# Kernel tuning notes

Measured on AMD Instinct MI355X. Metric: run time of the kernel, lower is better.

## Reference

```python
import jax, jax.numpy as jnp
import numpy as np

D_MODEL = 1024
NUM_HEADS = 16
HEAD_DIM = D_MODEL // NUM_HEADS  # 64
# NOTE: the torch module passes scale=attention_head_size (NOT 1/sqrt(dh));
# we reproduce that exact math: scores are MULTIPLIED by head_dim.
SCALE = float(HEAD_DIM)

B, S = 2, 2048


def setup_inputs() -> dict:
    key = jax.random.key(0)
    ks = jax.random.split(key, 6)
    q = jax.random.normal(ks[0], (B, S, D_MODEL), dtype=jnp.float32)
    k = jax.random.normal(ks[1], (B, S, D_MODEL), dtype=jnp.float32)
    v = jax.random.normal(ks[2], (B, S, D_MODEL), dtype=jnp.float32)
    # Linear weights stored as [in, out]; scaled like typical init so the
    # (head_dim-scaled) logits stay numerically sane.
    w_std = 0.02
    Wq = jax.random.normal(ks[3], (D_MODEL, D_MODEL), dtype=jnp.float32) * w_std
    Wk = jax.random.normal(ks[4], (D_MODEL, D_MODEL), dtype=jnp.float32) * w_std
    Wv = jax.random.normal(ks[5], (D_MODEL, D_MODEL), dtype=jnp.float32) * w_std
    return {"q": q, "k": k, "v": v, "Wq": Wq, "Wk": Wk, "Wv": Wv}


def reference(q, k, v, Wq, Wk, Wv):
    Bq, Sq, _ = q.shape
    # QKV projections (qkv_bias=False), split into heads: [B, S, H, dh]
    qh = (q @ Wq).reshape(Bq, Sq, NUM_HEADS, HEAD_DIM)
    kh = (k @ Wk).reshape(Bq, Sq, NUM_HEADS, HEAD_DIM)
    vh = (v @ Wv).reshape(Bq, Sq, NUM_HEADS, HEAD_DIM)
    # Full materialized scores [B, H, Sq, Sk] -- the naive MHA pattern.
    sims = jnp.einsum("bqhd,bkhd->bhqk", qh, kh) * SCALE
    attn = jax.nn.softmax(sims, axis=-1)
    # Second matmul, then merge heads back: [B, S, D]
    out = jnp.einsum("bhqk,bkhd->bqhd", attn, vh).reshape(Bq, Sq, D_MODEL)
    return out
```

## Files before the change

kernel.cpp:

```cpp
#include <hip/hip_runtime.h>
#include <cstdint>
#include <cstddef>

typedef unsigned short u16;
typedef __bf16 bf16x8 __attribute__((ext_vector_type(8)));
typedef float f32x4 __attribute__((ext_vector_type(4)));
typedef unsigned int u32x4 __attribute__((ext_vector_type(4)));
typedef unsigned int u32x2 __attribute__((ext_vector_type(2)));
typedef u16 u16x4 __attribute__((ext_vector_type(4)));

typedef __attribute__((address_space(3))) void lds_void;
typedef __attribute__((address_space(1))) void glb_void;

constexpr float CEXP = 92.33248261689366f;

constexpr size_t XSZ = 4096ull * 1024ull;
constexpr size_t WSZ = 1024ull * 1024ull;
constexpr size_t OFF_XQH = 0;
constexpr size_t OFF_XQL = OFF_XQH + XSZ;
constexpr size_t OFF_XKH = OFF_XQL + XSZ;
constexpr size_t OFF_XKL = OFF_XKH + XSZ;
constexpr size_t OFF_XVH = OFF_XKL + XSZ;
constexpr size_t OFF_XVL = OFF_XVH + XSZ;
constexpr size_t OFF_WQH = OFF_XVL + XSZ;
constexpr size_t OFF_WQL = OFF_WQH + WSZ;
constexpr size_t OFF_WKH = OFF_WQL + WSZ;
constexpr size_t OFF_WKL = OFF_WKH + WSZ;
constexpr size_t OFF_WVH = OFF_WKL + WSZ;
constexpr size_t OFF_WVL = OFF_WVH + WSZ;
constexpr size_t OFF_QH  = OFF_WVL + WSZ;
constexpr size_t OFF_QL  = OFF_QH + XSZ;
constexpr size_t OFF_KH  = OFF_QL + XSZ;
constexpr size_t OFF_KL  = OFF_KH + XSZ;
constexpr size_t OFF_VH  = OFF_KL + XSZ;
constexpr size_t OFF_VT  = OFF_VH + XSZ;

__device__ __forceinline__ u16 f2b(float f) {
  unsigned u = __builtin_bit_cast(unsigned, f);
  return (u16)((u + 0x7FFFu + ((u >> 16) & 1u)) >> 16);
}
__device__ __forceinline__ float b2f(u16 h) {
  return __builtin_bit_cast(float, ((unsigned)h) << 16);
}
__device__ __forceinline__ bf16x8 ld8(const u16* p) {
  return __builtin_bit_cast(bf16x8, *(const u32x4*)p);
}
__device__ __forceinline__ unsigned pk2(float a, float b) {
#if __has_builtin(__builtin_amdgcn_cvt_pk_bf16_f32)
  auto v = __builtin_amdgcn_cvt_pk_bf16_f32(a, b);
  return __builtin_bit_cast(unsigned, v);
#else
  return (unsigned)f2b(a) | ((unsigned)f2b(b) << 16);
#endif
}
__device__ __forceinline__ float ex2(float x) {
#if __has_builtin(__builtin_amdgcn_exp2f)
  return __builtin_amdgcn_exp2f(x);
#else
  return exp2f(x);
#endif
}
__device__ __forceinline__ void glds16(const u16* g, u16* l) {
  __builtin_amdgcn_global_load_lds((const glb_void*)g, (lds_void*)l, 16, 0, 0);
}
__device__ __forceinline__ int swz32(int row, int cg) {
  return row * 32 + ((cg ^ ((row >> 1) & 3)) * 8);
}
__device__ __forceinline__ int swz64(int row, int cg) {
  return row * 64 + ((cg ^ (row & 7)) * 8);
}

__global__ __launch_bounds__(256) void convert_all(const float* __restrict__ q,
                                                   const float* __restrict__ k,
                                                   const float* __restrict__ v,
                                                   const float* __restrict__ Wq,
                                                   const float* __restrict__ Wk,
                                                   const float* __restrict__ Wv,
                                                   u16* __restrict__ ws) {
  __shared__ float tile[32][33];
  int id = blockIdx.x;
  int t = threadIdx.x;
  if (id < 6144) {
    int z = id >> 11, blk = id & 2047;
    const float* in = (z == 0) ? q : (z == 1) ? k : v;
    u16* hi = ws + ((z == 0) ? OFF_XQH : (z == 1) ? OFF_XKH : OFF_XVH);
    u16* lo = ws + ((z == 0) ? OFF_XQL : (z == 1) ? OFF_XKL : OFF_XVL);
    size_t i = ((size_t)blk * 256u + t) * 8u;
    float4 v0 = *(const float4*)(in + i);
    float4 v1 = *(const float4*)(in + i + 4);
    float a[8] = {v0.x, v0.y, v0.z, v0.w, v1.x, v1.y, v1.z, v1.w};
    u16 hv[8], lv[8];
#pragma unroll
    for (int j = 0; j < 8; ++j) {
      u16 hb = f2b(a[j]);
      hv[j] = hb;
      lv[j] = f2b(a[j] - b2f(hb));
    }
    *(u32x4*)(hi + i) = *(const u32x4*)hv;
    if (z != 2) *(u32x4*)(lo + i) = *(const u32x4*)lv;
  } else {
    int r0 = id - 6144;
    int z = r0 >> 10, rem = r0 & 1023;
    const float* W = (z == 0) ? Wq : (z == 1) ? Wk : Wv;
    u16* hiT = ws + ((z == 0) ? OFF_WQH : (z == 1) ? OFF_WKH : OFF_WVH);
    u16* loT = ws + ((z == 0) ? OFF_WQL : (z == 1) ? OFF_WKL : OFF_WVL);
    int n0 = (rem & 31) * 32, k0 = (rem >> 5) * 32;
    int r = t >> 3, c0 = (t & 7) * 4;
    float4 vv = *(const float4*)(W + (size_t)(k0 + r) * 1024 + n0 + c0);
    tile[r][c0] = vv.x; tile[r][c0 + 1] = vv.y; tile[r][c0 + 2] = vv.z; tile[r][c0 + 3] = vv.w;
    __syncthreads();
    u16x4 hv, lv;
#pragma unroll
    for (int j = 0; j < 4; ++j) {
      float x = tile[c0 + j][r];
      u16 hb = f2b(x);
      hv[j] = hb;
      lv[j] = f2b(x - b2f(hb));
    }
    size_t o = (size_t)(n0 + r) * 1024 + k0 + c0;
    *(u16x4*)(hiT + o) = hv;
    if (z != 2) *(u16x4*)(loT + o) = lv;
  }
}

__global__ __launch_bounds__(256, 3) void gemm_qkv(u16* __restrict__ ws) {
  __shared__ u16 smem[16384];
  u16* sAh = smem;
  u16* sAl = smem + 4096;
  u16* sBh = smem + 8192;
  u16* sBl = smem + 12288;
  u16* cbuf = smem;

  int id = blockIdx.x;
  int xcd = id & 7, seq = id >> 3;
  int pair = (seq >> 3) * 8 + xcd;
  int tile_n = seq & 7;
  int z = pair >> 5;
  int tile_m = pair & 31;

  const u16 *Ah, *Al, *Bh, *Bl; u16 *Oh, *Ol; bool split;
  if (z == 0)      { Ah = ws + OFF_XQH; Al = ws + OFF_XQL; Bh = ws + OFF_WQH; Bl = ws + OFF_WQL; Oh = ws + OFF_QH; Ol = ws + OFF_QL; split = true; }
  else if (z == 1) { Ah = ws + OFF_XKH; Al = ws + OFF_XKL; Bh = ws + OFF_WKH; Bl = ws + OFF_WKL; Oh = ws + OFF_KH; Ol = ws + OFF_KL; split = true; }
  else             { Ah = ws + OFF_XVH; Al = nullptr;      Bh = ws + OFF_WVH; Bl = nullptr;      Oh = ws + OFF_VT; Ol = nullptr;    split = false; }
  float oscale = (z == 0) ? CEXP : 1.0f;
  int m0 = tile_m * 128, n0 = tile_n * 128;
  int t = threadIdx.x, lane = t & 63, wave = t >> 6;
  int quad = lane >> 4, l15 = lane & 15;
  int wm = (wave >> 1) * 64, wn = (wave & 1) * 64;
  int rl = lane >> 2, cgl = lane & 3;
  f32x4 acc[4][4] = {};

  size_t gA[2], gB[2]; int lb[2];
#pragma unroll
  for (int i = 0; i < 2; ++i) {
    int row = i * 64 + wave * 16 + rl;
    int gsw = (cgl ^ ((row >> 1) & 3)) * 8;
    gA[i] = (size_t)(m0 + row) * 1024 + gsw;
    gB[i] = (size_t)(n0 + row) * 1024 + gsw;
    lb[i] = i * 2048 + wave * 512;
  }

  for (int kb = 0; kb < 32; ++kb) {
    int k0 = kb * 32;
    __syncthreads();
#pragma unroll
    for (int i = 0; i < 2; ++i) {
      glds16(Ah + gA[i] + k0, &sAh[lb[i]]);
      if (split) glds16(Al + gA[i] + k0, &sAl[lb[i]]);
      glds16(Bh + gB[i] + k0, &sBh[lb[i]]);
      if (split) glds16(Bl + gB[i] + k0, &sBl[lb[i]]);
    }
    __syncthreads();
    bf16x8 afh[4], afl[4];
#pragma unroll
    for (int mt = 0; mt < 4; ++mt) {
      int ra = wm + mt * 16 + l15;
      afh[mt] = ld8(&sAh[swz32(ra, quad)]);
      if (split) afl[mt] = ld8(&sAl[swz32(ra, quad)]);
    }
#pragma unroll
    for (int nt = 0; nt < 4; ++nt) {
      int rb = wn + nt * 16 + l15;
      bf16x8 bfh = ld8(&sBh[swz32(rb, quad)]);
      bf16x8 bfl;
      if (split) bfl = ld8(&sBl[swz32(rb, quad)]);
#pragma unroll
      for (int mt = 0; mt < 4; ++mt) {
        acc[mt][nt] = __builtin_amdgcn_mfma_f32_16x16x32_bf16(afh[mt], bfh, acc[mt][nt], 0, 0, 0);
        if (split) {
          acc[mt][nt] = __builtin_amdgcn_mfma_f32_16x16x32_bf16(afl[mt], bfh, acc[mt][nt], 0, 0, 0);
          acc[mt][nt] = __builtin_amdgcn_mfma_f32_16x16x32_bf16(afh[mt], bfl, acc[mt][nt], 0, 0, 0);
        }
      }
    }
  }
  auto epi_round = [&](u16* dst, bool lo_round) {
#pragma unroll
    for (int mt = 0; mt < 4; ++mt)
#pragma unroll
      for (int nt = 0; nt < 4; ++nt)
#pragma unroll
        for (int r = 0; r < 4; ++r) {
          int row = wm + mt * 16 + quad * 4 + r;
          int col = wn + nt * 16 + l15;
          float v = acc[mt][nt][r] * oscale;
          u16 hb = f2b(v);
          u16 val = lo_round ? f2b(v - b2f(hb)) : hb;
          cbuf[row * 128 + (((col >> 3) ^ (row & 15)) * 8) + (col & 7)] = val;
        }
    __syncthreads();
#pragma unroll
    for (int rr = 0; rr < 2; ++rr) {
      int row = rr * 64 + (t >> 2), seg = t & 3;
      int gm = m0 + row, bb = gm >> 11, s = gm & 2047;
      int hh = (n0 >> 6) + (seg >> 1), d0 = (seg & 1) * 32;
      u16* gp = dst + ((size_t)(bb * 16 + hh) * 2048 + s) * 64 + d0;
#pragma unroll
      for (int i = 0; i < 4; ++i) {
        int phys = (seg * 4 + i) ^ (row & 15);
        *(u32x4*)(gp + i * 8) = *(const u32x4*)(&cbuf[row * 128 + phys * 8]);
      }
    }
  };
  __syncthreads();
  if (split) {
    epi_round(Oh, false);
    __syncthreads();
    epi_round(Ol, true);
  } else {
#pragma unroll
    for (int mt = 0; mt < 4; ++mt)
#pragma unroll
      for (int nt = 0; nt < 4; ++nt)
#pragma unroll
        for (int r = 0; r < 4; ++r) {
          int row = wm + mt * 16 + quad * 4 + r;
          int col = wn + nt * 16 + l15;
          cbuf[row * 128 + (((col >> 3) ^ (row & 15)) * 8) + (col & 7)] =
              f2b(acc[mt][nt][r]);
        }
    __syncthreads();
    int col = t >> 1, sh = t & 1;
    int hg = (n0 + col) >> 6, d = (n0 + col) & 63;
    int bb = m0 >> 11, s0 = m0 & 2047;
#pragma unroll
    for (int part = 0; part < 2; ++part) {
      u16 vals[32];
#pragma unroll
      for (int i = 0; i < 32; ++i) {
        int row = part * 64 + sh * 32 + i;
        vals[i] = cbuf[row * 128 + (((col >> 3) ^ (row & 15)) * 8) + (col & 7)];
      }
      u16* gp = Oh + ((size_t)((bb * 16 + hg) * 64 + d)) * 2048 + s0 + part * 64 + sh * 32;
#pragma unroll
      for (int i = 0; i < 4; ++i)
        *(u32x4*)(gp + i * 8) = *(const u32x4*)(&vals[i * 8]);
    }
  }
}

__global__ __launch_bounds__(256, 4) void attn(const u16* __restrict__ ws,
                                               float* __restrict__ out) {
  __shared__ u16 lkh[64 * 64];
  __shared__ u16 lkl[64 * 64];
  __shared__ u16 lvt[2][64 * 64];
  __shared__ u16 lp[4][16 * 64];
  const u16* Qh = ws + OFF_QH; const u16* Ql = ws + OFF_QL;
  const u16* Kh = ws + OFF_KH; const u16* Kl = ws + OFF_KL;
  const u16* Vt = ws + OFF_VT;
  int id = blockIdx.x;
  int xcd = id & 7, slot = id >> 3;
  int hh = xcd * 4 + (slot >> 5);
  int q0 = (slot & 31) * 64;
  int b = hh >> 4, h = hh & 15;
  int t = threadIdx.x, lane = t & 63, wave = t >> 6;
  int quad = lane >> 4, l15 = lane & 15;
  size_t hb = (size_t)hh * (2048 * 64);
  bf16x8 onesf;
#pragma unroll
  for (int j = 0; j < 8; ++j) onesf[j] = __builtin_bit_cast(__bf16, (u16)0x3F80);
  int qrow = q0 + wave * 16 + l15;
  bf16x8 qfh[2], qfl[2];
#pragma unroll
  for (int ks = 0; ks < 2; ++ks) {
    size_t qo = hb + (size_t)qrow * 64 + ks * 32 + quad * 8;
    qfh[ks] = ld8(Qh + qo);
    qfl[ks] = ld8(Ql + qo);
  }
  float mi = -1e30f;
  f32x4 lsum = {};
  f32x4 o[4] = {};
  int rl = lane >> 3, cgl = lane & 7;

  size_t aK[2], aV[2]; int lb[2];
#pragma unroll
  for (int i = 0; i < 2; ++i) {
    int row = wave * 16 + i * 8 + rl;
    int cgg = cgl ^ (row & 7);
    aK[i] = hb + (size_t)row * 64 + cgg * 8;
    aV[i] = hb + (size_t)row * 2048 + cgg * 8;
    lb[i] = (wave * 16 + i * 8) * 64;
  }
  int soF[2][4];
#pragma unroll
  for (int ks = 0; ks < 2; ++ks)
#pragma unroll
    for (int nt = 0; nt < 4; ++nt)
      soF[ks][nt] = swz64(nt * 16 + l15, ks * 4 + quad);
  int soP[4];
  {
    int r7 = l15 & 7;
#pragma unroll
    for (int nt = 0; nt < 4; ++nt) {
      int c = nt * 2 + (quad >> 1);
      soP[nt] = l15 * 64 + ((c ^ r7) * 8) + (quad & 1) * 4;
    }
  }
  int soPa[2];
#pragma unroll
  for (int ks = 0; ks < 2; ++ks) soPa[ks] = swz64(l15, ks * 4 + quad);
  u16* lpw = &lp[wave][0];

#pragma unroll
  for (int i = 0; i < 2; ++i) {
    glds16(Kh + aK[i], &lkh[lb[i]]);
    glds16(Kl + aK[i], &lkl[lb[i]]);
    glds16(Vt + aV[i], &lvt[0][lb[i]]);
  }
  u32x4 pk_[2], pl_[2], pv_[2];
#pragma unroll
  for (int i = 0; i < 2; ++i) {
    pk_[i] = *(const u32x4*)(Kh + aK[i] + 4096);
    pl_[i] = *(const u32x4*)(Kl + aK[i] + 4096);
    pv_[i] = *(const u32x4*)(Vt + aV[i] + 64);
  }
  __syncthreads();

  for (int kt = 0; kt < 32; ++kt) {
    f32x4 sc[4] = {};
    __builtin_amdgcn_s_setprio(1);
#pragma unroll
    for (int nt = 0; nt < 4; ++nt) {
#pragma unroll
      for (int ks = 0; ks < 2; ++ks) {
        bf16x8 kh_ = ld8(&lkh[soF[ks][nt]]);
        bf16x8 kl_ = ld8(&lkl[soF[ks][nt]]);
        sc[nt] = __builtin_amdgcn_mfma_f32_16x16x32_bf16(kh_, qfh[ks], sc[nt], 0, 0, 0);
        sc[nt] = __builtin_amdgcn_mfma_f32_16x16x32_bf16(kl_, qfh[ks], sc[nt], 0, 0, 0);
        sc[nt] = __builtin_amdgcn_mfma_f32_16x16x32_bf16(kh_, qfl[ks], sc[nt], 0, 0, 0);
      }
    }
    __builtin_amdgcn_s_setprio(0);
    __syncthreads();
    if (kt < 31) {
#pragma unroll
      for (int i = 0; i < 2; ++i) {
        *(u32x4*)(&lkh[lb[i] + lane * 8]) = pk_[i];
        *(u32x4*)(&lkl[lb[i] + lane * 8]) = pl_[i];
        *(u32x4*)(&lvt[(kt + 1) & 1][lb[i] + lane * 8]) = pv_[i];
      }
    }
    __syncthreads();
    if (kt < 30) {
#pragma unroll
      for (int i = 0; i < 2; ++i) {
        pk_[i] = *(const u32x4*)(Kh + aK[i] + (kt + 2) * 4096);
        pl_[i] = *(const u32x4*)(Kl + aK[i] + (kt + 2) * 4096);
        pv_[i] = *(const u32x4*)(Vt + aV[i] + (kt + 2) * 64);
      }
    }
    float t0 = fmaxf(fmaxf(sc[0][0], sc[0][1]), sc[0][2]);
    float t1 = fmaxf(fmaxf(sc[0][3], sc[1][0]), sc[1][1]);
    float t2 = fmaxf(fmaxf(sc[1][2], sc[1][3]), sc[2][0]);
    float t3 = fmaxf(fmaxf(sc[2][1], sc[2][2]), sc[2][3]);
    float t4 = fmaxf(fmaxf(sc[3][0], sc[3][1]), sc[3][2]);
    float mx = fmaxf(fmaxf(fmaxf(t0, t1), fmaxf(t2, t3)), fmaxf(t4, sc[3][3]));
    mx = fmaxf(mx, __shfl_xor(mx, 16));
    mx = fmaxf(mx, __shfl_xor(mx, 32));
    float mi_old = mi;
    unsigned long long live = __ballot(mx > mi_old - 28.0f);
    float mn = fmaxf(mi_old, mx);
    mi = mn;
    if (live) {
      unsigned long long grew = __ballot(mx > mi_old);
#pragma unroll
      for (int nt = 0; nt < 4; ++nt) {
        unsigned u01 = pk2(ex2(sc[nt][0] - mn), ex2(sc[nt][1] - mn));
        unsigned u23 = pk2(ex2(sc[nt][2] - mn), ex2(sc[nt][3] - mn));
        *(u32x2*)(&lpw[soP[nt]]) = u32x2{u01, u23};
      }
      if (grew) {
        float a = ex2(mi_old - mn);
#pragma unroll
        for (int r = 0; r < 4; ++r) {
          lsum[r] *= a;
          o[0][r] *= a; o[1][r] *= a; o[2][r] *= a; o[3][r] *= a;
        }
      }
      asm volatile("s_waitcnt lgkmcnt(0)" ::: "memory");
      bf16x8 pa[2];
#pragma unroll
      for (int ks = 0; ks < 2; ++ks) pa[ks] = ld8(&lpw[soPa[ks]]);
      __builtin_amdgcn_s_setprio(1);
      lsum = __builtin_amdgcn_mfma_f32_16x16x32_bf16(onesf, pa[0], lsum, 0, 0, 0);
      lsum = __builtin_amdgcn_mfma_f32_16x16x32_bf16(onesf, pa[1], lsum, 0, 0, 0);
      const u16* lv = &lvt[kt & 1][0];
#pragma unroll
      for (int nt = 0; nt < 4; ++nt)
#pragma unroll
        for (int ks = 0; ks < 2; ++ks) {
          bf16x8 bv = ld8(&lv[soF[ks][nt]]);
          o[nt] = __builtin_amdgcn_mfma_f32_16x16x32_bf16(bv, pa[ks], o[nt], 0, 0, 0);
        }
      __builtin_amdgcn_s_setprio(0);
    }
  }
  float inv = 1.0f / lsum[0];
  float* op = out + (size_t)(b * 2048 + q0 + wave * 16 + l15) * 1024 + h * 64;
#pragma unroll
  for (int nt = 0; nt < 4; ++nt) {
    f32x4 w;
#pragma unroll
    for (int r = 0; r < 4; ++r) w[r] = o[nt][r] * inv;
    *(f32x4*)(op + nt * 16 + quad * 4) = w;
  }
}

extern "C" void kernel_launch(void* const* d_in, const int* in_sizes, int n_in,
                              void* d_out, int out_size, void* d_ws, size_t ws_size,
                              hipStream_t stream) {
  const float* q  = (const float*)d_in[0];
  const float* k  = (const float*)d_in[1];
  const float* v  = (const float*)d_in[2];
  const float* Wq = (const float*)d_in[3];
  const float* Wk = (const float*)d_in[4];
  const float* Wv = (const float*)d_in[5];
  u16* ws = (u16*)d_ws;
  float* out = (float*)d_out;

  convert_all<<<9216, 256, 0, stream>>>(q, k, v, Wq, Wk, Wv, ws);
  gemm_qkv<<<768, 256, 0, stream>>>(ws);
  attn<<<1024, 256, 0, stream>>>(ws, out);
}
```

Before: 269.9 us.

## Fuse fp32 activation split-to-bf16 conversion into QKV GEMM tile loads

Removes the separate pass that converted q/k/v activations to hi/lo bf16 in workspace. The GEMM now loads fp32 activation tiles directly into LDS, using a new XOR swizzle, and builds the hi/lo bf16 fragments in registers before the MFMAs. This saves the write and re-read of roughly 48 MB of intermediate activations. In exchange, each tile moves twice the fp32 bytes into LDS and the inner loop gains conversion ALU work. Each N tile of the same rows also repeats that conversion.

Result: no change. 272.7 us (+1.0%).

```diff
diff --git a/kernel.cpp b/kernel.cpp
--- a/kernel.cpp
+++ b/kernel.cpp
@@ -16,13 +16,7 @@
 
 constexpr size_t XSZ = 4096ull * 1024ull;
 constexpr size_t WSZ = 1024ull * 1024ull;
-constexpr size_t OFF_XQH = 0;
-constexpr size_t OFF_XQL = OFF_XQH + XSZ;
-constexpr size_t OFF_XKH = OFF_XQL + XSZ;
-constexpr size_t OFF_XKL = OFF_XKH + XSZ;
-constexpr size_t OFF_XVH = OFF_XKL + XSZ;
-constexpr size_t OFF_XVL = OFF_XVH + XSZ;
-constexpr size_t OFF_WQH = OFF_XVL + XSZ;
+constexpr size_t OFF_WQH = 0;
 constexpr size_t OFF_WQL = OFF_WQH + WSZ;
 constexpr size_t OFF_WKH = OFF_WQL + WSZ;
 constexpr size_t OFF_WKL = OFF_WKH + WSZ;
@@ -32,8 +26,7 @@
 constexpr size_t OFF_QL  = OFF_QH + XSZ;
 constexpr size_t OFF_KH  = OFF_QL + XSZ;
 constexpr size_t OFF_KL  = OFF_KH + XSZ;
-constexpr size_t OFF_VH  = OFF_KL + XSZ;
-constexpr size_t OFF_VT  = OFF_VH + XSZ;
+constexpr size_t OFF_VT  = OFF_KL + XSZ;
 
 __device__ __forceinline__ u16 f2b(float f) {
   unsigned u = __builtin_bit_cast(unsigned, f);
@@ -41,6 +34,9 @@
 }
 __device__ __forceinline__ float b2f(u16 h) {
   return __builtin_bit_cast(float, ((unsigned)h) << 16);
+}
+__device__ __forceinline__ float bitf(unsigned u) {
+  return __builtin_bit_cast(float, u);
 }
 __device__ __forceinline__ bf16x8 ld8(const u16* p) {
   return __builtin_bit_cast(bf16x8, *(const u32x4*)p);
@@ -60,7 +56,7 @@
   return exp2f(x);
 #endif
 }
-__device__ __forceinline__ void glds16(const u16* g, u16* l) {
+__device__ __forceinline__ void glds16(const void* g, void* l) {
   __builtin_amdgcn_global_load_lds((const glb_void*)g, (lds_void*)l, 16, 0, 0);
 }
 __device__ __forceinline__ int swz32(int row, int cg) {
@@ -70,63 +66,41 @@
   return row * 64 + ((cg ^ (row & 7)) * 8);
 }
 
-__global__ __launch_bounds__(256) void convert_all(const float* __restrict__ q,
-                                                   const float* __restrict__ k,
-                                                   const float* __restrict__ v,
-                                                   const float* __restrict__ Wq,
-                                                   const float* __restrict__ Wk,
-                                                   const float* __restrict__ Wv,
-                                                   u16* __restrict__ ws) {
+__global__ __launch_bounds__(256) void convert_w(const float* __restrict__ Wq,
+                                                 const float* __restrict__ Wk,
+                                                 const float* __restrict__ Wv,
+                                                 u16* __restrict__ ws) {
   __shared__ float tile[32][33];
   int id = blockIdx.x;
   int t = threadIdx.x;
-  if (id < 6144) {
-    int z = id >> 11, blk = id & 2047;
-    const float* in = (z == 0) ? q : (z == 1) ? k : v;
-    u16* hi = ws + ((z == 0) ? OFF_XQH : (z == 1) ? OFF_XKH : OFF_XVH);
-    u16* lo = ws + ((z == 0) ? OFF_XQL : (z == 1) ? OFF_XKL : OFF_XVL);
-    size_t i = ((size_t)blk * 256u + t) * 8u;
-    float4 v0 = *(const float4*)(in + i);
-    float4 v1 = *(const float4*)(in + i + 4);
-    float a[8] = {v0.x, v0.y, v0.z, v0.w, v1.x, v1.y, v1.z, v1.w};
-    u16 hv[8], lv[8];
-#pragma unroll
-    for (int j = 0; j < 8; ++j) {
-      u16 hb = f2b(a[j]);
-      hv[j] = hb;
-      lv[j] = f2b(a[j] - b2f(hb));
-    }
-    *(u32x4*)(hi + i) = *(const u32x4*)hv;
-    if (z != 2) *(u32x4*)(lo + i) = *(const u32x4*)lv;
-  } else {
-    int r0 = id - 6144;
-    int z = r0 >> 10, rem = r0 & 1023;
-    const float* W = (z == 0) ? Wq : (z == 1) ? Wk : Wv;
-    u16* hiT = ws + ((z == 0) ? OFF_WQH : (z == 1) ? OFF_WKH : OFF_WVH);
-    u16* loT = ws + ((z == 0) ? OFF_WQL : (z == 1) ? OFF_WKL : OFF_WVL);
-    int n0 = (rem & 31) * 32, k0 = (rem >> 5) * 32;
-    int r = t >> 3, c0 = (t & 7) * 4;
-    float4 vv = *(const float4*)(W + (size_t)(k0 + r) * 1024 + n0 + c0);
-    tile[r][c0] = vv.x; tile[r][c0 + 1] = vv.y; tile[r][c0 + 2] = vv.z; tile[r][c0 + 3] = vv.w;
-    __syncthreads();
-    u16x4 hv, lv;
-#pragma unroll
-    for (int j = 0; j < 4; ++j) {
-      float x = tile[c0 + j][r];
-      u16 hb = f2b(x);
-      hv[j] = hb;
-      lv[j] = f2b(x - b2f(hb));
-    }
-    size_t o = (size_t)(n0 + r) * 1024 + k0 + c0;
-    *(u16x4*)(hiT + o) = hv;
-    if (z != 2) *(u16x4*)(loT + o) = lv;
-  }
-}
-
-__global__ __launch_bounds__(256, 3) void gemm_qkv(u16* __restrict__ ws) {
+  int z = id >> 10, rem = id & 1023;
+  const float* W = (z == 0) ? Wq : (z == 1) ? Wk : Wv;
+  u16* hiT = ws + ((z == 0) ? OFF_WQH : (z == 1) ? OFF_WKH : OFF_WVH);
+  u16* loT = ws + ((z == 0) ? OFF_WQL : (z == 1) ? OFF_WKL : OFF_WVL);
+  int n0 = (rem & 31) * 32, k0 = (rem >> 5) * 32;
+  int r = t >> 3, c0 = (t & 7) * 4;
+  float4 vv = *(const float4*)(W + (size_t)(k0 + r) * 1024 + n0 + c0);
+  tile[r][c0] = vv.x; tile[r][c0 + 1] = vv.y; tile[r][c0 + 2] = vv.z; tile[r][c0 + 3] = vv.w;
+  __syncthreads();
+  u16x4 hv, lv;
+#pragma unroll
+  for (int j = 0; j < 4; ++j) {
+    float x = tile[c0 + j][r];
+    u16 hb = f2b(x);
+    hv[j] = hb;
+    lv[j] = f2b(x - b2f(hb));
+  }
+  size_t o = (size_t)(n0 + r) * 1024 + k0 + c0;
+  *(u16x4*)(hiT + o) = hv;
+  if (z != 2) *(u16x4*)(loT + o) = lv;
+}
+
+__global__ __launch_bounds__(256, 3) void gemm_qkv(u16* __restrict__ ws,
+                                                   const float* __restrict__ xq,
+                                                   const float* __restrict__ xk,
+                                                   const float* __restrict__ xv) {
   __shared__ u16 smem[16384];
-  u16* sAh = smem;
-  u16* sAl = smem + 4096;
+  float* sAf = (float*)smem;
   u16* sBh = smem + 8192;
   u16* sBl = smem + 12288;
   u16* cbuf = smem;
@@ -138,45 +112,71 @@
   int z = pair >> 5;
   int tile_m = pair & 31;
 
-  const u16 *Ah, *Al, *Bh, *Bl; u16 *Oh, *Ol; bool split;
-  if (z == 0)      { Ah = ws + OFF_XQH; Al = ws + OFF_XQL; Bh = ws + OFF_WQH; Bl = ws + OFF_WQL; Oh = ws + OFF_QH; Ol = ws + OFF_QL; split = true; }
-  else if (z == 1) { Ah = ws + OFF_XKH; Al = ws + OFF_XKL; Bh = ws + OFF_WKH; Bl = ws + OFF_WKL; Oh = ws + OFF_KH; Ol = ws + OFF_KL; split = true; }
-  else             { Ah = ws + OFF_XVH; Al = nullptr;      Bh = ws + OFF_WVH; Bl = nullptr;      Oh = ws + OFF_VT; Ol = nullptr;    split = false; }
+  const float* X = (z == 0) ? xq : (z == 1) ? xk : xv;
+  const u16 *Bh, *Bl; u16 *Oh, *Ol; bool split;
+  if (z == 0)      { Bh = ws + OFF_WQH; Bl = ws + OFF_WQL; Oh = ws + OFF_QH; Ol = ws + OFF_QL; split = true; }
+  else if (z == 1) { Bh = ws + OFF_WKH; Bl = ws + OFF_WKL; Oh = ws + OFF_KH; Ol = ws + OFF_KL; split = true; }
+  else             { Bh = ws + OFF_WVH; Bl = nullptr;      Oh = ws + OFF_VT; Ol = nullptr;    split = false; }
   float oscale = (z == 0) ? CEXP : 1.0f;
   int m0 = tile_m * 128, n0 = tile_n * 128;
   int t = threadIdx.x, lane = t & 63, wave = t >> 6;
   int quad = lane >> 4, l15 = lane & 15;
   int wm = (wave >> 1) * 64, wn = (wave & 1) * 64;
   int rl = lane >> 2, cgl = lane & 3;
+  int rt = t >> 3, ct = t & 7;
   f32x4 acc[4][4] = {};
 
-  size_t gA[2], gB[2]; int lb[2];
+  size_t gAf[4]; int lbAf[4];
+#pragma unroll
+  for (int i = 0; i < 4; ++i) {
+    int row = i * 32 + rt;
+    gAf[i] = (size_t)(m0 + row) * 1024 + ((ct ^ (row & 7)) * 4);
+    lbAf[i] = (i * 256 + t) * 4;
+  }
+  size_t gB[2]; int lbB[2];
 #pragma unroll
   for (int i = 0; i < 2; ++i) {
-    int row = i * 64 + wave * 16 + rl;
-    int gsw = (cgl ^ ((row >> 1) & 3)) * 8;
-    gA[i] = (size_t)(m0 + row) * 1024 + gsw;
-    gB[i] = (size_t)(n0 + row) * 1024 + gsw;
-    lb[i] = i * 2048 + wave * 512;
+    int rowB = wave * 32 + i * 16 + rl;
+    gB[i] = (size_t)(n0 + rowB) * 1024 + (cgl ^ ((rowB >> 1) & 3)) * 8;
+    lbB[i] = wave * 1024 + i * 512;
+  }
+  int soAf[4][2];
+#pragma unroll
+  for (int mt = 0; mt < 4; ++mt) {
+    int ra = wm + mt * 16 + l15;
+    soAf[mt][0] = ra * 32 + (((2 * quad) ^ (ra & 7)) * 4);
+    soAf[mt][1] = ra * 32 + (((2 * quad + 1) ^ (ra & 7)) * 4);
   }
 
   for (int kb = 0; kb < 32; ++kb) {
     int k0 = kb * 32;
     __syncthreads();
 #pragma unroll
+    for (int i = 0; i < 4; ++i)
+      glds16(X + gAf[i] + k0, sAf + lbAf[i]);
+#pragma unroll
     for (int i = 0; i < 2; ++i) {
-      glds16(Ah + gA[i] + k0, &sAh[lb[i]]);
-      if (split) glds16(Al + gA[i] + k0, &sAl[lb[i]]);
-      glds16(Bh + gB[i] + k0, &sBh[lb[i]]);
-      if (split) glds16(Bl + gB[i] + k0, &sBl[lb[i]]);
+      glds16(Bh + gB[i] + k0, &sBh[lbB[i]]);
+      if (split) glds16(Bl + gB[i] + k0, &sBl[lbB[i]]);
     }
     __syncthreads();
     bf16x8 afh[4], afl[4];
 #pragma unroll
     for (int mt = 0; mt < 4; ++mt) {
-      int ra = wm + mt * 16 + l15;
-      afh[mt] = ld8(&sAh[swz32(ra, quad)]);
-      if (split) afl[mt] = ld8(&sAl[swz32(ra, quad)]);
+      f32x4 a0 = *(const f32x4*)(sAf + soAf[mt][0]);
+      f32x4 a1 = *(const f32x4*)(sAf + soAf[mt][1]);
+      u32x4 hw;
+      hw[0] = pk2(a0[0], a0[1]); hw[1] = pk2(a0[2], a0[3]);
+      hw[2] = pk2(a1[0], a1[1]); hw[3] = pk2(a1[2], a1[3]);
+      afh[mt] = __builtin_bit_cast(bf16x8, hw);
+      if (split) {
+        u32x4 lw;
+        lw[0] = pk2(a0[0] - bitf(hw[0] << 16), a0[1] - bitf(hw[0] & 0xFFFF0000u));
+        lw[1] = pk2(a0[2] - bitf(hw[1] << 16), a0[3] - bitf(hw[1] & 0xFFFF0000u));
+        lw[2] = pk2(a1[0] - bitf(hw[2] << 16), a1[1] - bitf(hw[2] & 0xFFFF0000u));
+        lw[3] = pk2(a1[2] - bitf(hw[3] << 16), a1[3] - bitf(hw[3] & 0xFFFF0000u));
+        afl[mt] = __builtin_bit_cast(bf16x8, lw);
+      }
     }
 #pragma unroll
     for (int nt = 0; nt < 4; ++nt) {
@@ -438,7 +438,7 @@
   u16* ws = (u16*)d_ws;
   float* out = (float*)d_out;
 
-  convert_all<<<9216, 256, 0, stream>>>(q, k, v, Wq, Wk, Wv, ws);
-  gemm_qkv<<<768, 256, 0, stream>>>(ws);
+  convert_w<<<3072, 256, 0, stream>>>(Wq, Wk, Wv, ws);
+  gemm_qkv<<<768, 256, 0, stream>>>(ws, q, k, v);
   attn<<<1024, 256, 0, stream>>>(ws, out);
 }
```
